# Optimization experiments

Measured on AMD Instinct MI355X. Metric: run time of the kernel, lower is better.

## Reference

```python
import jax, jax.numpy as jnp
import numpy as np

N = 50000          # nodes
E = 800000         # edges (before self-loops)
F_IN = 256         # feature_dim
HEADS = 3
OUT = 128          # per-head channels
HO = HEADS * OUT   # 384
NUM_GRAPHS = 64
NUM_CLASSES = 2
SLOPE = 0.2        # PyG GATConv default negative_slope


def setup_inputs() -> dict:
    key = jax.random.key(0)
    ks = jax.random.split(key, 8)
    x = jax.random.normal(ks[0], (N, F_IN), dtype=jnp.float32)
    edge_index = jax.random.randint(ks[1], (2, E), 0, N)
    batch = jnp.sort(jax.random.randint(ks[2], (N,), 0, NUM_GRAPHS))
    # GATConv params (glorot-ish scales)
    W = jax.random.normal(ks[3], (F_IN, HO), dtype=jnp.float32) * (1.0 / np.sqrt(F_IN))
    att_src = jax.random.normal(ks[4], (HEADS, OUT), dtype=jnp.float32) * 0.1
    att_dst = jax.random.normal(ks[5], (HEADS, OUT), dtype=jnp.float32) * 0.1
    bias = jnp.zeros((HO,), dtype=jnp.float32)
    fc_w = jax.random.normal(ks[6], (HO, NUM_CLASSES), dtype=jnp.float32) * 0.05
    fc_b = jnp.zeros((NUM_CLASSES,), dtype=jnp.float32)
    return {"x": x, "edge_index": edge_index, "batch": batch, "W": W,
            "att_src": att_src, "att_dst": att_dst, "bias": bias,
            "fc_w": fc_w, "fc_b": fc_b}


def reference(x, edge_index, batch, W, att_src, att_dst, bias, fc_w, fc_b):
    n = x.shape[0]
    h = (x @ W).reshape(n, HEADS, OUT)                      # [N, H, C]
    # add self-loops (PyG default add_self_loops=True)
    loops = jnp.arange(n)
    src = jnp.concatenate([edge_index[0], loops])           # [E+N]
    dst = jnp.concatenate([edge_index[1], loops])
    # per-node attention logits
    a_src = jnp.einsum('nhc,hc->nh', h, att_src)            # [N, H]
    a_dst = jnp.einsum('nhc,hc->nh', h, att_dst)
    e = jax.nn.leaky_relu(a_src[src] + a_dst[dst], SLOPE)   # [E+N, H]
    # segment softmax over incoming edges of each dst node
    emax = jax.ops.segment_max(e, dst, num_segments=n)
    ex = jnp.exp(e - emax[dst])
    denom = jax.ops.segment_sum(ex, dst, num_segments=n)
    alpha = ex / (denom[dst] + 1e-16)                       # [E+N, H]
    # weighted scatter-add aggregation
    msg = h[src] * alpha[:, :, None]                        # [E+N, H, C]
    out = jax.ops.segment_sum(msg, dst, num_segments=n)     # [N, H, C]
    out = jax.nn.relu(out.reshape(n, HO) + bias)            # [N, 384]
    # global mean pool per graph
    counts = jax.ops.segment_sum(jnp.ones((n,), out.dtype), batch,
                                 num_segments=NUM_GRAPHS)
    pooled = jax.ops.segment_sum(out, batch, num_segments=NUM_GRAPHS)
    pooled = pooled / jnp.maximum(counts, 1.0)[:, None]     # [G, 384]
    return pooled @ fc_w + fc_b                             # [G, num_classes]
```

## Files before the change

kernel.cpp:

```cpp
#include <hip/hip_runtime.h>
#include <hip/hip_bf16.h>
#include <math.h>

#define HEADS 3
#define HO 384
#define NGRAPH 64
#define F_IN 256
#define SLOPE 0.2f

typedef __attribute__((ext_vector_type(8))) short bf8;
typedef __attribute__((ext_vector_type(4))) float f4;
typedef __attribute__((ext_vector_type(2))) unsigned u2v;
typedef __attribute__((ext_vector_type(4))) unsigned u4v;

__device__ __forceinline__ unsigned short bfr(float f) {
    unsigned u = __float_as_uint(f);
    u += 0x7fffu + ((u >> 16) & 1u);
    return (unsigned short)(u >> 16);
}
__device__ __forceinline__ float bflo(unsigned u) { return __uint_as_float(u << 16); }
__device__ __forceinline__ float bfhi(unsigned u) { return __uint_as_float(u & 0xffff0000u); }
__device__ __forceinline__ float lrelu(float v) { return (v > 0.f) ? v : SLOPE * v; }

__device__ __forceinline__ void mix2(float& a0, float& a1, unsigned h2, float wm) {
    asm("v_fma_mix_f32 %0, %2, %3, %0 op_sel:[0,0,0] op_sel_hi:[1,0,0]\n\t"
        "v_fma_mix_f32 %1, %2, %3, %1 op_sel:[1,0,0] op_sel_hi:[1,0,0]"
        : "+v"(a0), "+v"(a1)
        : "v"(h2), "v"(wm));
}
__device__ __forceinline__ void dec8_mix(float* acc, float wm, unsigned ux, unsigned uy,
                                         unsigned c64) {
    unsigned p0 = __builtin_amdgcn_perm(ux, c64, 0x00050004u);
    unsigned p1 = __builtin_amdgcn_perm(ux, c64, 0x00070006u);
    unsigned p2 = __builtin_amdgcn_perm(uy, c64, 0x00050004u);
    unsigned p3 = __builtin_amdgcn_perm(uy, c64, 0x00070006u);
    mix2(acc[0], acc[1], p0, wm);
    mix2(acc[2], acc[3], p1, wm);
    mix2(acc[4], acc[5], p2, wm);
    mix2(acc[6], acc[7], p3, wm);
}

__global__ __launch_bounds__(256) void misc_k(const int* __restrict__ ei,
                                              const float* __restrict__ W,
                                              const int* __restrict__ batch,
                                              int* __restrict__ count,
                                              int* __restrict__ rank,
                                              short* __restrict__ WbT,
                                              int* __restrict__ gstart,
                                              int NBc, int E, int N) {
    int b = blockIdx.x;
    if (b < NBc) {
        int e = b * 256 + threadIdx.x;
        int ET = E + N;
        if (e >= ET) return;
        int d = (e < E) ? ei[E + e] : (e - E);
        rank[e] = atomicAdd(&count[d], 1);
    } else if (b < NBc + 384) {
        int n = b - NBc;
        int k = threadIdx.x;
        WbT[n * 256 + k] = (short)bfr(W[(size_t)k * HO + n]);
    } else {
        int g = threadIdx.x;
        if (g > NGRAPH) return;
        int lo = 0, hi = N;
        while (lo < hi) { int mid = (lo + hi) >> 1; if (batch[mid] < g) lo = mid + 1; else hi = mid; }
        gstart[g] = lo;
    }
}

#define XS_STRIDE 40
__global__ __launch_bounds__(256, 3) void gemm_att(const float* __restrict__ X,
                                                   const short* __restrict__ WbT,
                                                   const float* __restrict__ att_src,
                                                   const float* __restrict__ att_dst,
                                                   unsigned char* __restrict__ hc,
                                                   float* __restrict__ ni,
                                                   float* __restrict__ aDstO, int N) {
    __shared__ short Xs[64 * XS_STRIDE];
    __shared__ short Bs[384 * XS_STRIDE];
    __shared__ float lsS[64][8];
    __shared__ float lsD[64][8];
    __shared__ float lsM[64][8];
    __shared__ float sclS[64][4];
    int t = threadIdx.x;
    int w = t >> 6, lane = t & 63;
    int quad = lane >> 4, l15 = lane & 15;
    int rbase = blockIdx.x * 64;

    int sr = t >> 2;
    int sko = (t & 3) * 8;
    int xrow = rbase + sr;
    xrow = (xrow < N) ? xrow : (N - 1);
    const float* xrp = X + (size_t)xrow * F_IN;

    f4 acc[4][6] = {};

    float4 p0 = *(const float4*)(xrp + sko);
    float4 p1 = *(const float4*)(xrp + sko + 4);

    for (int k0 = 0; k0 < F_IN; k0 += 32) {
        __syncthreads();
        {
            bf8 pk;
            pk[0] = (short)bfr(p0.x); pk[1] = (short)bfr(p0.y);
            pk[2] = (short)bfr(p0.z); pk[3] = (short)bfr(p0.w);
            pk[4] = (short)bfr(p1.x); pk[5] = (short)bfr(p1.y);
            pk[6] = (short)bfr(p1.z); pk[7] = (short)bfr(p1.w);
            *(bf8*)(&Xs[sr * XS_STRIDE + sko]) = pk;
        }
#pragma unroll
        for (int i = 0; i < 6; i++) {
            int n = i * 64 + sr;
            bf8 b = *(const bf8*)(WbT + (size_t)n * F_IN + k0 + sko);
            *(bf8*)(&Bs[n * XS_STRIDE + sko]) = b;
        }
        __syncthreads();
        if (k0 + 32 < F_IN) {
            p0 = *(const float4*)(xrp + k0 + 32 + sko);
            p1 = *(const float4*)(xrp + k0 + 32 + sko + 4);
        }
        bf8 ar[4], br[6];
#pragma unroll
        for (int at = 0; at < 4; at++)
            ar[at] = *(const bf8*)(&Xs[(at * 16 + l15) * XS_STRIDE + quad * 8]);
#pragma unroll
        for (int nt = 0; nt < 6; nt++)
            br[nt] = *(const bf8*)(&Bs[(w * 96 + nt * 16 + l15) * XS_STRIDE + quad * 8]);
#pragma unroll
        for (int at = 0; at < 4; at++)
#pragma unroll
            for (int nt = 0; nt < 6; nt++)
                acc[at][nt] = __builtin_amdgcn_mfma_f32_16x16x32_bf16(ar[at], br[nt], acc[at][nt], 0, 0, 0);
    }

    const int splits[4] = {6, 2, 4, 0};
    int split = splits[w];
    float asv[6], adv[6];
#pragma unroll
    for (int nt = 0; nt < 6; nt++) {
        int c = w * 96 + nt * 16 + l15;
        asv[nt] = att_src[c];
        adv[nt] = att_dst[c];
    }
#pragma unroll
    for (int at = 0; at < 4; at++) {
#pragma unroll
        for (int r = 0; r < 4; r++) {
            float paS = 0.f, pbS = 0.f, paD = 0.f, pbD = 0.f;
#pragma unroll
            for (int nt = 0; nt < 6; nt++) {
                float v = acc[at][nt][r];
                if (nt < split) { paS += v * asv[nt]; paD += v * adv[nt]; }
                else            { pbS += v * asv[nt]; pbD += v * adv[nt]; }
            }
#pragma unroll
            for (int off = 1; off < 16; off <<= 1) {
                paS += __shfl_xor(paS, off); pbS += __shfl_xor(pbS, off);
                paD += __shfl_xor(paD, off); pbD += __shfl_xor(pbD, off);
            }
            if (l15 == 0) {
                int row = at * 16 + quad * 4 + r;
                lsS[row][w * 2 + 0] = paS; lsS[row][w * 2 + 1] = pbS;
                lsD[row][w * 2 + 0] = paD; lsD[row][w * 2 + 1] = pbD;
            }
        }
    }
#pragma unroll
    for (int at = 0; at < 4; at++) {
#pragma unroll
        for (int r = 0; r < 4; r++) {
            float pa = 0.f, pb = 0.f;
#pragma unroll
            for (int nt = 0; nt < 6; nt++) {
                float v = fabsf(acc[at][nt][r]);
                if (nt < split) pa = fmaxf(pa, v); else pb = fmaxf(pb, v);
            }
#pragma unroll
            for (int off = 1; off < 16; off <<= 1) {
                pa = fmaxf(pa, __shfl_xor(pa, off));
                pb = fmaxf(pb, __shfl_xor(pb, off));
            }
            if (l15 == 0) {
                int row = at * 16 + quad * 4 + r;
                lsM[row][w * 2 + 0] = pa; lsM[row][w * 2 + 1] = pb;
            }
        }
    }
    __syncthreads();
    if (t < 64) {
        float s0 = fmaxf(lsM[t][0], lsM[t][2]);
        float s1 = fmaxf(lsM[t][3], lsM[t][4]);
        float s2 = fmaxf(lsM[t][5], lsM[t][7]);
        sclS[t][0] = (s0 > 0.f) ? 127.f / s0 : 0.f;
        sclS[t][1] = (s1 > 0.f) ? 127.f / s1 : 0.f;
        sclS[t][2] = (s2 > 0.f) ? 127.f / s2 : 0.f;
        int node = rbase + t;
        if (node < N) {
            aDstO[node * 3 + 0] = lsD[t][0] + lsD[t][2];
            aDstO[node * 3 + 1] = lsD[t][3] + lsD[t][4];
            aDstO[node * 3 + 2] = lsD[t][5] + lsD[t][7];
            float4 nA, nB;
            nA.x = lsS[t][0] + lsS[t][2];
            nA.y = lsS[t][3] + lsS[t][4];
            nA.z = lsS[t][5] + lsS[t][7];
            nA.w = s0 / 127.f;
            nB.x = s1 / 127.f;
            nB.y = s2 / 127.f;
            nB.z = 0.f; nB.w = 0.f;
            *(float4*)(ni + (size_t)node * 8) = nA;
            *(float4*)(ni + (size_t)node * 8 + 4) = nB;
        }
    }
    __syncthreads();
#pragma unroll
    for (int at = 0; at < 4; at++) {
#pragma unroll
        for (int nt = 0; nt < 6; nt++) {
            int hd = (w * 96 + nt * 16) >> 7;
#pragma unroll
            for (int r = 0; r < 4; r++) {
                int row = at * 16 + quad * 4 + r;
                int node = rbase + row;
                float rq = sclS[row][hd];
                int qi = (int)rintf(acc[at][nt][r] * rq) + 128;
                if (node < N) hc[(size_t)node * 384 + w * 96 + nt * 16 + l15] = (unsigned char)qi;
            }
        }
    }
}

__global__ __launch_bounds__(256) void scan_a(const int* __restrict__ count,
                                              int* __restrict__ offsets,
                                              int* __restrict__ bsums, int N) {
    __shared__ int tmp[256];
    int t = threadIdx.x;
    int i = blockIdx.x * 256 + t;
    int v = (i < N) ? count[i] : 0;
    tmp[t] = v;
    __syncthreads();
    for (int off = 1; off < 256; off <<= 1) {
        int x = (t >= off) ? tmp[t - off] : 0;
        __syncthreads();
        tmp[t] += x;
        __syncthreads();
    }
    if (i < N) offsets[i] = tmp[t] - v;
    if (t == 255) bsums[blockIdx.x] = tmp[255];
}

__global__ __launch_bounds__(256) void scan_b(int* __restrict__ bsums, int NB) {
    __shared__ int tmp[256];
    int t = threadIdx.x;
    int v = (t < NB) ? bsums[t] : 0;
    tmp[t] = v;
    __syncthreads();
    for (int off = 1; off < 256; off <<= 1) {
        int x = (t >= off) ? tmp[t - off] : 0;
        __syncthreads();
        tmp[t] += x;
        __syncthreads();
    }
    if (t < NB) bsums[t] = tmp[t] - v;
}

__global__ __launch_bounds__(256) void scan_c(int* __restrict__ offsets,
                                              const int* __restrict__ bsums, int N) {
    int i = blockIdx.x * 256 + threadIdx.x;
    if (i < N) offsets[i] += bsums[blockIdx.x];
}

__global__ __launch_bounds__(256) void scatter_k(const int* __restrict__ ei,
                                                 const int* __restrict__ rank,
                                                 const int* __restrict__ offsets,
                                                 int* __restrict__ csr_src, int E, int N) {
    int e = blockIdx.x * 256 + threadIdx.x;
    int ET = E + N;
    if (e >= ET) return;
    int s, d;
    if (e < E) { s = ei[e]; d = ei[E + e]; } else { s = e - E; d = s; }
    csr_src[offsets[d] + rank[e]] = s;
}

__global__ __launch_bounds__(256) void aggregate_k(const unsigned* __restrict__ hcw,
                                                   const int* __restrict__ csr_src,
                                                   const int* __restrict__ offsets,
                                                   const int* __restrict__ count,
                                                   const float* __restrict__ ni,
                                                   const float* __restrict__ a_dst,
                                                   const float* __restrict__ bias,
                                                   unsigned* __restrict__ outb, int N) {
    __shared__ float ws[4][3][68];
    __shared__ int   si[4][64];
    int wv = threadIdx.x >> 6;
    int wid = blockIdx.x * 4 + wv;
    int lane = threadIdx.x & 63;
    if (wid >= N) return;
    int start = offsets[wid], n = count[wid];
    float ad0 = a_dst[wid * 3 + 0], ad1 = a_dst[wid * 3 + 1], ad2 = a_dst[wid * 3 + 2];
    int hm = (lane < 48) ? (lane >> 4) : 0;
    int off = (lane < 48) ? 2 * lane : 0;
    float acc[8] = {0.f, 0.f, 0.f, 0.f, 0.f, 0.f, 0.f, 0.f};
    float wsum = 0.f;
    float i0, i1, i2;
    const unsigned c64 = 0x64646464u;

    if (n <= 64) {
        int sreg = 0;
        float l0 = -INFINITY, l1 = -INFINITY, l2 = -INFINITY;
        float s0v = 0.f, s1v = 0.f, s2v = 0.f;
        if (lane < n) {
            sreg = csr_src[start + lane];
            float4 A = *(const float4*)(ni + (size_t)sreg * 8);
            float4 B = *(const float4*)(ni + (size_t)sreg * 8 + 4);
            l0 = lrelu(A.x + ad0); l1 = lrelu(A.y + ad1); l2 = lrelu(A.z + ad2);
            s0v = A.w; s1v = B.x; s2v = B.y;
        }
        float m0 = l0, m1 = l1, m2 = l2;
#pragma unroll
        for (int o = 1; o < 64; o <<= 1) {
            m0 = fmaxf(m0, __shfl_xor(m0, o));
            m1 = fmaxf(m1, __shfl_xor(m1, o));
            m2 = fmaxf(m2, __shfl_xor(m2, o));
        }
        float e0 = (lane < n) ? expf(l0 - m0) : 0.f;
        float e1 = (lane < n) ? expf(l1 - m1) : 0.f;
        float e2 = (lane < n) ? expf(l2 - m2) : 0.f;
        float s0 = e0, s1 = e1, s2 = e2;
#pragma unroll
        for (int o = 1; o < 64; o <<= 1) {
            s0 += __shfl_xor(s0, o);
            s1 += __shfl_xor(s1, o);
            s2 += __shfl_xor(s2, o);
        }
        i0 = 1.f / (s0 + 1e-16f); i1 = 1.f / (s1 + 1e-16f); i2 = 1.f / (s2 + 1e-16f);
        ws[wv][0][lane] = e0 * s0v;
        ws[wv][1][lane] = e1 * s1v;
        ws[wv][2][lane] = e2 * s2v;
        si[wv][lane] = sreg;
        __builtin_amdgcn_wave_barrier();

        for (int j = 0; j < n; j += 8) {
            int4 ia = *(const int4*)&si[wv][j];
            int4 ib = *(const int4*)&si[wv][j + 4];
            u2v u0 = *(const u2v*)(hcw + (size_t)ia.x * 96 + off);
            u2v u1 = *(const u2v*)(hcw + (size_t)ia.y * 96 + off);
            u2v u2 = *(const u2v*)(hcw + (size_t)ia.z * 96 + off);
            u2v u3 = *(const u2v*)(hcw + (size_t)ia.w * 96 + off);
            u2v u4 = *(const u2v*)(hcw + (size_t)ib.x * 96 + off);
            u2v u5 = *(const u2v*)(hcw + (size_t)ib.y * 96 + off);
            u2v u6 = *(const u2v*)(hcw + (size_t)ib.z * 96 + off);
            u2v u7 = *(const u2v*)(hcw + (size_t)ib.w * 96 + off);
            float4 wa = *(const float4*)&ws[wv][hm][j];
            float4 wb = *(const float4*)&ws[wv][hm][j + 4];
            wsum += (wa.x + wa.y + wa.z + wa.w) + (wb.x + wb.y + wb.z + wb.w);
            dec8_mix(acc, wa.x, u0.x, u0.y, c64);
            dec8_mix(acc, wa.y, u1.x, u1.y, c64);
            dec8_mix(acc, wa.z, u2.x, u2.y, c64);
            dec8_mix(acc, wa.w, u3.x, u3.y, c64);
            dec8_mix(acc, wb.x, u4.x, u4.y, c64);
            dec8_mix(acc, wb.y, u5.x, u5.y, c64);
            dec8_mix(acc, wb.z, u6.x, u6.y, c64);
            dec8_mix(acc, wb.w, u7.x, u7.y, c64);
        }
    } else {
        float m0 = -INFINITY, m1 = -INFINITY, m2 = -INFINITY;
        for (int j = lane; j < n; j += 64) {
            int s = csr_src[start + j];
            float4 A = *(const float4*)(ni + (size_t)s * 8);
            m0 = fmaxf(m0, lrelu(A.x + ad0));
            m1 = fmaxf(m1, lrelu(A.y + ad1));
            m2 = fmaxf(m2, lrelu(A.z + ad2));
        }
#pragma unroll
        for (int o = 1; o < 64; o <<= 1) {
            m0 = fmaxf(m0, __shfl_xor(m0, o));
            m1 = fmaxf(m1, __shfl_xor(m1, o));
            m2 = fmaxf(m2, __shfl_xor(m2, o));
        }
        float s0 = 0.f, s1 = 0.f, s2 = 0.f;
        for (int j = lane; j < n; j += 64) {
            int s = csr_src[start + j];
            float4 A = *(const float4*)(ni + (size_t)s * 8);
            s0 += expf(lrelu(A.x + ad0) - m0);
            s1 += expf(lrelu(A.y + ad1) - m1);
            s2 += expf(lrelu(A.z + ad2) - m2);
        }
#pragma unroll
        for (int o = 1; o < 64; o <<= 1) {
            s0 += __shfl_xor(s0, o);
            s1 += __shfl_xor(s1, o);
            s2 += __shfl_xor(s2, o);
        }
        i0 = 1.f / (s0 + 1e-16f); i1 = 1.f / (s1 + 1e-16f); i2 = 1.f / (s2 + 1e-16f);
        for (int j = 0; j < n; j++) {
            int s = csr_src[start + j];
            float4 A = *(const float4*)(ni + (size_t)s * 8);
            float4 B = *(const float4*)(ni + (size_t)s * 8 + 4);
            float w0 = expf(lrelu(A.x + ad0) - m0) * A.w;
            float w1 = expf(lrelu(A.y + ad1) - m1) * B.x;
            float w2 = expf(lrelu(A.z + ad2) - m2) * B.y;
            float wm = (hm == 0) ? w0 : ((hm == 1) ? w1 : w2);
            u2v u = *(const u2v*)(hcw + (size_t)s * 96 + off);
            wsum += wm;
            dec8_mix(acc, wm, u.x, u.y, c64);
        }
    }

    if (lane < 48) {
        float im = (hm == 0) ? i0 : ((hm == 1) ? i1 : i2);
        float corr = 1152.f * wsum;
        float4 b0 = *(const float4*)(bias + 8 * lane);
        float4 b1 = *(const float4*)(bias + 8 * lane + 4);
        float bb[8] = {b0.x, b0.y, b0.z, b0.w, b1.x, b1.y, b1.z, b1.w};
        u4v pk;
#pragma unroll
        for (int j = 0; j < 4; j++) {
            float x0 = (acc[2 * j] - corr) * im + bb[2 * j];
            float x1 = (acc[2 * j + 1] - corr) * im + bb[2 * j + 1];
            x0 = (x0 > 0.f) ? x0 : 0.f;
            x1 = (x1 > 0.f) ? x1 : 0.f;
            pk[j] = (unsigned)bfr(x0) | ((unsigned)bfr(x1) << 16);
        }
        *(u4v*)(outb + (size_t)wid * 192 + 4 * lane) = pk;
    }
}

__global__ __launch_bounds__(192) void pool_k(const unsigned* __restrict__ outb,
                                              const int* __restrict__ gstart,
                                              float* __restrict__ pooled) {
    int g = blockIdx.x;
    int chunk = blockIdx.y;
    int t = threadIdx.x;
    int lo = gstart[g], hi = gstart[g + 1];
    float al = 0.f, ah = 0.f;
    for (int r = lo + chunk; r < hi; r += 8) {
        unsigned u = outb[(size_t)r * 192 + t];
        al += bflo(u);
        ah += bfhi(u);
    }
    atomicAdd(&pooled[g * HO + 2 * t], al);
    atomicAdd(&pooled[g * HO + 2 * t + 1], ah);
}

__global__ __launch_bounds__(64) void fc_k(const float* __restrict__ pooled,
                                           const int* __restrict__ gstart,
                                           const float* __restrict__ fc_w,
                                           const float* __restrict__ fc_b,
                                           float* __restrict__ out) {
    int g = blockIdx.x;
    int lane = threadIdx.x;
    float a0 = 0.f, a1 = 0.f;
#pragma unroll
    for (int k = 0; k < 6; k++) {
        int c = lane + 64 * k;
        float pv = pooled[g * HO + c];
        a0 += pv * fc_w[c * 2 + 0];
        a1 += pv * fc_w[c * 2 + 1];
    }
#pragma unroll
    for (int off = 32; off > 0; off >>= 1) {
        a0 += __shfl_down(a0, off);
        a1 += __shfl_down(a1, off);
    }
    if (lane == 0) {
        float cnt = fmaxf((float)(gstart[g + 1] - gstart[g]), 1.0f);
        out[g * 2 + 0] = a0 / cnt + fc_b[0];
        out[g * 2 + 1] = a1 / cnt + fc_b[1];
    }
}

extern "C" void kernel_launch(void* const* d_in, const int* in_sizes, int n_in,
                              void* d_out, int out_size, void* d_ws, size_t ws_size,
                              hipStream_t stream) {
    const float* x       = (const float*)d_in[0];
    const int*   ei      = (const int*)d_in[1];
    const int*   batch   = (const int*)d_in[2];
    const float* W       = (const float*)d_in[3];
    const float* att_src = (const float*)d_in[4];
    const float* att_dst = (const float*)d_in[5];
    const float* bias    = (const float*)d_in[6];
    const float* fc_w    = (const float*)d_in[7];
    const float* fc_b    = (const float*)d_in[8];
    float* out = (float*)d_out;

    const int N = in_sizes[2];
    const int E = in_sizes[1] / 2;
    const int ET = E + N;

    char* p = (char*)d_ws;
    auto alloc = [&](size_t bytes) -> char* {
        char* r = p;
        p += (bytes + 255) & ~(size_t)255;
        return r;
    };
    short*         wbt    = (short*)alloc((size_t)HO * F_IN * 2);
    unsigned char* hc     = (unsigned char*)alloc((size_t)N * 384);
    unsigned*      outb   = (unsigned*)alloc((size_t)N * 192 * 4);
    float*         ni     = (float*)alloc((size_t)N * 8 * 4);
    float*         a_dst  = (float*)alloc((size_t)N * 3 * 4);
    char*          zstart = p;
    int*           count  = (int*)alloc((size_t)N * 4);
    float*         pooled = (float*)alloc((size_t)NGRAPH * HO * 4);
    size_t         zbytes = (size_t)(p - zstart);
    int*           offsets = (int*)alloc((size_t)N * 4);
    int*           rank    = (int*)alloc((size_t)ET * 4);
    int*           bsums   = (int*)alloc(4096);
    int*           gstart  = (int*)alloc(1024);
    int*           csr_src = (int*)alloc((size_t)ET * 4);

    hipMemsetAsync(zstart, 0, zbytes, stream);

    int NBc = (ET + 255) / 256;
    misc_k<<<NBc + 384 + 1, 256, 0, stream>>>(ei, W, batch, count, rank, wbt, gstart,
                                              NBc, E, N);
    gemm_att<<<(N + 63) / 64, 256, 0, stream>>>(x, wbt, att_src, att_dst,
                                                hc, ni, a_dst, N);
    int NB = (N + 255) / 256;
    scan_a<<<NB, 256, 0, stream>>>(count, offsets, bsums, N);
    scan_b<<<1, 256, 0, stream>>>(bsums, NB);
    scan_c<<<NB, 256, 0, stream>>>(offsets, bsums, N);
    scatter_k<<<(ET + 255) / 256, 256, 0, stream>>>(ei, rank, offsets, csr_src, E, N);
    aggregate_k<<<(N + 3) / 4, 256, 0, stream>>>((const unsigned*)hc, csr_src, offsets,
                                                 count, ni, a_dst, bias, outb, N);
    dim3 pg(NGRAPH, 8);
    pool_k<<<pg, 192, 0, stream>>>(outb, gstart, pooled);
    fc_k<<<NGRAPH, 64, 0, stream>>>(pooled, gstart, fc_w, fc_b, out);

    (void)n_in; (void)out_size; (void)ws_size;
}
```

Baseline: 298.2 us.

## Pre-convert X to bf16 and load GEMM operands straight from global memory

Moves the fp32-to-bf16 conversion of X into the misc preprocessing kernel, writing a bf16 copy to workspace. The GEMM then drops LDS staging and barriers and loads MFMA fragments directly from global memory, relying on cache for the shared W tiles. Launch bounds drop to 2 blocks per SM to allow more registers. In exchange there is an extra pass that writes and rereads a bf16 copy of X, plus uncoalesced 16-byte per-lane global loads in the inner loop.

```diff
diff --git a/kernel.cpp b/kernel.cpp
--- a/kernel.cpp
+++ b/kernel.cpp
@@ -43,9 +43,11 @@
 __global__ __launch_bounds__(256) void misc_k(const int* __restrict__ ei,
                                               const float* __restrict__ W,
                                               const int* __restrict__ batch,
+                                              const float* __restrict__ X,
                                               int* __restrict__ count,
                                               int* __restrict__ rank,
                                               short* __restrict__ WbT,
+                                              short* __restrict__ Xb,
                                               int* __restrict__ gstart,
                                               int NBc, int E, int N) {
     int b = blockIdx.x;
@@ -59,25 +61,34 @@
         int n = b - NBc;
         int k = threadIdx.x;
         WbT[n * 256 + k] = (short)bfr(W[(size_t)k * HO + n]);
-    } else {
+    } else if (b == NBc + 384) {
         int g = threadIdx.x;
         if (g > NGRAPH) return;
         int lo = 0, hi = N;
         while (lo < hi) { int mid = (lo + hi) >> 1; if (batch[mid] < g) lo = mid + 1; else hi = mid; }
         gstart[g] = lo;
-    }
-}
-
-#define XS_STRIDE 40
-__global__ __launch_bounds__(256, 3) void gemm_att(const float* __restrict__ X,
+    } else {
+        size_t base = (size_t)(b - (NBc + 385)) * 2048 + threadIdx.x * 8;
+        if (base + 8 <= (size_t)N * F_IN) {
+            float4 q0 = *(const float4*)(X + base);
+            float4 q1 = *(const float4*)(X + base + 4);
+            bf8 pk;
+            pk[0] = (short)bfr(q0.x); pk[1] = (short)bfr(q0.y);
+            pk[2] = (short)bfr(q0.z); pk[3] = (short)bfr(q0.w);
+            pk[4] = (short)bfr(q1.x); pk[5] = (short)bfr(q1.y);
+            pk[6] = (short)bfr(q1.z); pk[7] = (short)bfr(q1.w);
+            *(bf8*)(Xb + base) = pk;
+        }
+    }
+}
+
+__global__ __launch_bounds__(256, 2) void gemm_att(const short* __restrict__ Xb,
                                                    const short* __restrict__ WbT,
                                                    const float* __restrict__ att_src,
                                                    const float* __restrict__ att_dst,
                                                    unsigned char* __restrict__ hc,
                                                    float* __restrict__ ni,
                                                    float* __restrict__ aDstO, int N) {
-    __shared__ short Xs[64 * XS_STRIDE];
-    __shared__ short Bs[384 * XS_STRIDE];
     __shared__ float lsS[64][8];
     __shared__ float lsD[64][8];
     __shared__ float lsM[64][8];
@@ -87,45 +98,25 @@
     int quad = lane >> 4, l15 = lane & 15;
     int rbase = blockIdx.x * 64;
 
-    int sr = t >> 2;
-    int sko = (t & 3) * 8;
-    int xrow = rbase + sr;
-    xrow = (xrow < N) ? xrow : (N - 1);
-    const float* xrp = X + (size_t)xrow * F_IN;
-
     f4 acc[4][6] = {};
-
-    float4 p0 = *(const float4*)(xrp + sko);
-    float4 p1 = *(const float4*)(xrp + sko + 4);
-
+    const short* ap[4];
+#pragma unroll
+    for (int at = 0; at < 4; at++) {
+        int r = rbase + at * 16 + l15;
+        r = (r < N) ? r : (N - 1);
+        ap[at] = Xb + (size_t)r * F_IN + quad * 8;
+    }
+    const short* bp = WbT + (size_t)(w * 96 + l15) * F_IN + quad * 8;
+
+#pragma unroll
     for (int k0 = 0; k0 < F_IN; k0 += 32) {
-        __syncthreads();
-        {
-            bf8 pk;
-            pk[0] = (short)bfr(p0.x); pk[1] = (short)bfr(p0.y);
-            pk[2] = (short)bfr(p0.z); pk[3] = (short)bfr(p0.w);
-            pk[4] = (short)bfr(p1.x); pk[5] = (short)bfr(p1.y);
-            pk[6] = (short)bfr(p1.z); pk[7] = (short)bfr(p1.w);
-            *(bf8*)(&Xs[sr * XS_STRIDE + sko]) = pk;
-        }
-#pragma unroll
-        for (int i = 0; i < 6; i++) {
-            int n = i * 64 + sr;
-            bf8 b = *(const bf8*)(WbT + (size_t)n * F_IN + k0 + sko);
-            *(bf8*)(&Bs[n * XS_STRIDE + sko]) = b;
-        }
-        __syncthreads();
-        if (k0 + 32 < F_IN) {
-            p0 = *(const float4*)(xrp + k0 + 32 + sko);
-            p1 = *(const float4*)(xrp + k0 + 32 + sko + 4);
-        }
         bf8 ar[4], br[6];
 #pragma unroll
         for (int at = 0; at < 4; at++)
-            ar[at] = *(const bf8*)(&Xs[(at * 16 + l15) * XS_STRIDE + quad * 8]);
+            ar[at] = *(const bf8*)(ap[at] + k0);
 #pragma unroll
         for (int nt = 0; nt < 6; nt++)
-            br[nt] = *(const bf8*)(&Bs[(w * 96 + nt * 16 + l15) * XS_STRIDE + quad * 8]);
+            br[nt] = *(const bf8*)(bp + nt * 16 * F_IN + k0);
 #pragma unroll
         for (int at = 0; at < 4; at++)
 #pragma unroll
@@ -494,6 +485,7 @@
         return r;
     };
     short*         wbt    = (short*)alloc((size_t)HO * F_IN * 2);
+    short*         xb     = (short*)alloc((size_t)N * F_IN * 2);
     unsigned char* hc     = (unsigned char*)alloc((size_t)N * 384);
     unsigned*      outb   = (unsigned*)alloc((size_t)N * 192 * 4);
     float*         ni     = (float*)alloc((size_t)N * 8 * 4);
@@ -511,9 +503,10 @@
     hipMemsetAsync(zstart, 0, zbytes, stream);
 
     int NBc = (ET + 255) / 256;
-    misc_k<<<NBc + 384 + 1, 256, 0, stream>>>(ei, W, batch, count, rank, wbt, gstart,
-                                              NBc, E, N);
-    gemm_att<<<(N + 63) / 64, 256, 0, stream>>>(x, wbt, att_src, att_dst,
+    int NXc = (int)(((size_t)N * F_IN + 2047) / 2048);
+    misc_k<<<NBc + 384 + 1 + NXc, 256, 0, stream>>>(ei, W, batch, x, count, rank,
+                                                    wbt, xb, gstart, NBc, E, N);
+    gemm_att<<<(N + 63) / 64, 256, 0, stream>>>(xb, wbt, att_src, att_dst,
                                                 hc, ni, a_dst, N);
     int NB = (N + 255) / 256;
     scan_a<<<NB, 256, 0, stream>>>(count, offsets, bsums, N);
```

Result: slower. 309.1 us (+3.6%).
